# Kernel tuning notes

Hardware: AMD Instinct MI355X
Metric: run time of the kernel (lower is better)

Reference implementation:

```python
import jax, jax.numpy as jnp
import numpy as np


def setup_inputs() -> dict:
    key = jax.random.key(0)
    k1, k2, k3 = jax.random.split(key, 3)
    T, N, D = 128, 2048, 256  # snapshots, nodes, nhid
    inputs = jax.random.normal(k1, (T, N, D), dtype=jnp.float32)
    # torch init: uniform_(-0.1, 0.1)
    weight_W = jax.random.uniform(k2, (D, D), dtype=jnp.float32, minval=-0.1, maxval=0.1)
    weight_proj = jax.random.uniform(k3, (D, 1), dtype=jnp.float32, minval=-0.1, maxval=0.1)
    return {"inputs": inputs, "weight_W": weight_W, "weight_proj": weight_proj,
            "attention_width": 3}


def reference(inputs, weight_W, weight_proj, attention_width):
    # inputs: (T, N, D). For i < w the slice passes through unchanged.
    # For i >= w: window = inputs[i-w:i] (excludes position i),
    #   u = tanh(window @ W)            -> (w, N, D)
    #   a = (u @ proj).squeeze(-1)      -> (w, N)
    #   a = softmax over dim=1 (NODES)  -- legacy nn.Softmax() on 2D input
    #   out_i = sum_w a[...,None] * window -> (N, D)
    T, N, D = inputs.shape
    w = attention_width
    # windows for positions i = w .. T-1: (T-w, w, N, D)
    idx = jnp.arange(T - w)[:, None] + jnp.arange(w)[None, :]
    wins = inputs[idx]
    u = jnp.tanh(jnp.einsum('twnd,de->twne', wins, weight_W))  # (T-w, w, N, D)
    a = jnp.einsum('twnd,d->twn', u, weight_proj[:, 0])        # (T-w, w, N)
    a = jax.nn.softmax(a, axis=2)  # softmax across nodes (faithful to nn.Softmax())
    out = jnp.einsum('twn,twnd->tnd', a, wins)                 # (T-w, N, D)
    return jnp.concatenate([inputs[:w], out], axis=0)          # (T, N, D)
```

## Files before the change

kernel.cpp:

```cpp
#include <hip/hip_runtime.h>
#include <hip/hip_bf16.h>


#define T_DIM 128
#define N_DIM 2048
#define D_DIM 256
#define TS 127
#define M_TOT (TS * N_DIM)
#define BM 256
#define TB 32

typedef __attribute__((ext_vector_type(8))) short bf16x8;
typedef __attribute__((ext_vector_type(4))) float f32x4;

__device__ inline short f2bf(float f) {
  union { float f; unsigned u; } v; v.f = f;
  unsigned r = v.u + 0x7FFFu + ((v.u >> 16) & 1u);
  return (short)(r >> 16);
}

__device__ inline bf16x8 cvt8(const float4 a, const float4 b) {
  bf16x8 r;
  r[0] = f2bf(a.x); r[1] = f2bf(a.y); r[2] = f2bf(a.z); r[3] = f2bf(a.w);
  r[4] = f2bf(b.x); r[5] = f2bf(b.y); r[6] = f2bf(b.z); r[7] = f2bf(b.w);
  return r;
}

__device__ inline float fast_tanh(float x) {
  float e = __expf(fminf(2.0f * x, 30.0f));
  return __fdividef(e - 1.0f, e + 1.0f);
}

__global__ __launch_bounds__(256) void prep_kernel(const float* __restrict__ W,
                                                   short* __restrict__ Wt) {
  int id = blockIdx.x * 256 + threadIdx.x;
  int d = id >> 8;
  int e = id & 255;
  Wt[e * 256 + d] = f2bf(W[d * 256 + e]);
}

__global__ __launch_bounds__(512) void gemm_s_kernel(const float* __restrict__ x,
                                                     const short* __restrict__ Wt,
                                                     const float* __restrict__ proj,
                                                     float* __restrict__ s) {
  __shared__ short Ws[256 * 128];

  const int tid = threadIdx.x;
  const int lane = tid & 63;
  const int w = tid >> 6;
  const int quad = lane >> 4;
  const int l15 = lane & 15;
  const int m0 = blockIdx.x * BM;
  const size_t row0 = (size_t)(m0 + w * 32 + l15);
  const float* xp = x + row0 * D_DIM + quad * 8;
  const int swzc = (l15 & 7) << 4;

  float4 A0[2][2], A1[2][2];
  A0[0][0] = *(const float4*)(xp);
  A0[0][1] = *(const float4*)(xp + 4);
  A0[1][0] = *(const float4*)(xp + 16 * D_DIM);
  A0[1][1] = *(const float4*)(xp + 16 * D_DIM + 4);
  A1[0][0] = *(const float4*)(xp + 32);
  A1[0][1] = *(const float4*)(xp + 36);
  A1[1][0] = *(const float4*)(xp + 32 + 16 * D_DIM);
  A1[1][1] = *(const float4*)(xp + 36 + 16 * D_DIM);

  f32x4 acc[2][16] = {};

#pragma unroll
  for (int half = 0; half < 2; ++half) {
    if (half) __syncthreads();
#pragma unroll
    for (int it = 0; it < 8; ++it) {
      int slot = tid + it * 512;
      int e = slot >> 4;
      int ks = slot & 15;
      uint4 v = *(const uint4*)(Wt + e * D_DIM + half * 128 + ks * 8);
      int dst = (e * 256 + ks * 16) ^ ((e & 7) << 4);
      *(uint4*)((char*)Ws + dst) = v;
    }
    __syncthreads();

#pragma unroll
    for (int kt = 0; kt < 4; ++kt) {
      const int kg = half * 4 + kt;
      bf16x8 a0, a1;
      if ((kg & 1) == 0) {
        a0 = cvt8(A0[0][0], A0[0][1]);
        a1 = cvt8(A0[1][0], A0[1][1]);
        if (kg < 6) {
          const float* q = xp + (kg + 2) * 32;
          A0[0][0] = *(const float4*)(q);
          A0[0][1] = *(const float4*)(q + 4);
          A0[1][0] = *(const float4*)(q + 16 * D_DIM);
          A0[1][1] = *(const float4*)(q + 16 * D_DIM + 4);
        }
      } else {
        a0 = cvt8(A1[0][0], A1[0][1]);
        a1 = cvt8(A1[1][0], A1[1][1]);
        if (kg < 6) {
          const float* q = xp + (kg + 2) * 32;
          A1[0][0] = *(const float4*)(q);
          A1[0][1] = *(const float4*)(q + 4);
          A1[1][0] = *(const float4*)(q + 16 * D_DIM);
          A1[1][1] = *(const float4*)(q + 16 * D_DIM + 4);
        }
      }
      const int kb = (kt * 64 + quad * 16) ^ swzc;
#pragma unroll
      for (int ef = 0; ef < 16; ++ef) {
        const bf16x8 b =
            *(const bf16x8*)((const char*)Ws + (ef * 16 + l15) * 256 + kb);
        acc[0][ef] = __builtin_amdgcn_mfma_f32_16x16x32_bf16(a0, b, acc[0][ef], 0, 0, 0);
        acc[1][ef] = __builtin_amdgcn_mfma_f32_16x16x32_bf16(a1, b, acc[1][ef], 0, 0, 0);
      }
    }
  }

  float pj[16];
#pragma unroll
  for (int ef = 0; ef < 16; ++ef) pj[ef] = proj[ef * 16 + l15];

#pragma unroll
  for (int mf = 0; mf < 2; ++mf) {
#pragma unroll
    for (int r = 0; r < 4; ++r) {
      float val = 0.f;
#pragma unroll
      for (int ef = 0; ef < 16; ++ef)
        val = __builtin_fmaf(fast_tanh(acc[mf][ef][r]), pj[ef], val);
#pragma unroll
      for (int off = 1; off < 16; off <<= 1) val += __shfl_xor(val, off);
      if (l15 == 0) s[m0 + w * 32 + mf * 16 + quad * 4 + r] = val;
    }
  }
}

__global__ __launch_bounds__(256) void softmax_kernel(const float* __restrict__ s,
                                                      float* __restrict__ p) {
  const int t = blockIdx.x;
  const int tid = threadIdx.x;
  const float* row = s + (size_t)t * N_DIM;
  float v[8];
  float mx = -1e30f;
#pragma unroll
  for (int k = 0; k < 8; ++k) {
    v[k] = row[tid + k * 256];
    mx = fmaxf(mx, v[k]);
  }
#pragma unroll
  for (int off = 1; off < 64; off <<= 1) mx = fmaxf(mx, __shfl_xor(mx, off));
  __shared__ float redm[4];
  if ((tid & 63) == 0) redm[tid >> 6] = mx;
  __syncthreads();
  mx = fmaxf(fmaxf(redm[0], redm[1]), fmaxf(redm[2], redm[3]));

  float sum = 0.f;
#pragma unroll
  for (int k = 0; k < 8; ++k) {
    v[k] = __expf(v[k] - mx);
    sum += v[k];
  }
#pragma unroll
  for (int off = 1; off < 64; off <<= 1) sum += __shfl_xor(sum, off);
  __shared__ float reds[4];
  if ((tid & 63) == 0) reds[tid >> 6] = sum;
  __syncthreads();
  sum = reds[0] + reds[1] + reds[2] + reds[3];
  float inv = 1.0f / sum;
#pragma unroll
  for (int k = 0; k < 8; ++k) p[(size_t)t * N_DIM + tid + k * 256] = v[k] * inv;
}

__global__ __launch_bounds__(256) void out_kernel(const float* __restrict__ x,
                                                  const float* __restrict__ p,
                                                  float* __restrict__ out) {
  const int gid = blockIdx.x * 256 + threadIdx.x;
  const int n = gid >> 6;
  const int d4 = gid & 63;
  const int t0 = blockIdx.y * TB;
  const size_t base = (size_t)n * D_DIM + d4 * 4;
  const size_t tstride = (size_t)N_DIM * D_DIM;

  float4 x0 = {}, x1 = {}, x2 = {};
  float p0 = 0.f, p1 = 0.f, p2 = 0.f;
  if (t0 >= 3) {
    x0 = *(const float4*)(x + (t0 - 3) * tstride + base);
    x1 = *(const float4*)(x + (t0 - 2) * tstride + base);
    x2 = *(const float4*)(x + (t0 - 1) * tstride + base);
    p0 = p[(size_t)(t0 - 3) * N_DIM + n];
    p1 = p[(size_t)(t0 - 2) * N_DIM + n];
    p2 = p[(size_t)(t0 - 1) * N_DIM + n];
  }
  for (int t = t0; t < t0 + TB; ++t) {
    const float4 xc = *(const float4*)(x + t * tstride + base);
    const float pc = (t < TS) ? p[(size_t)t * N_DIM + n] : 0.f;
    float4 o;
    if (t >= 3) {
      o.x = p0 * x0.x + p1 * x1.x + p2 * x2.x;
      o.y = p0 * x0.y + p1 * x1.y + p2 * x2.y;
      o.z = p0 * x0.z + p1 * x1.z + p2 * x2.z;
      o.w = p0 * x0.w + p1 * x1.w + p2 * x2.w;
    } else {
      o = xc;
    }
    *(float4*)(out + t * tstride + base) = o;
    x0 = x1; x1 = x2; x2 = xc;
    p0 = p1; p1 = p2; p2 = pc;
  }
}

extern "C" void kernel_launch(void* const* d_in, const int* in_sizes, int n_in,
                              void* d_out, int out_size, void* d_ws, size_t ws_size,
                              hipStream_t stream) {
  const float* x = (const float*)d_in[0];
  const float* W = (const float*)d_in[1];
  const float* proj = (const float*)d_in[2];
  float* out = (float*)d_out;

  char* ws = (char*)d_ws;
  short* Wt = (short*)ws;
  float* s = (float*)(ws + 131072);
  float* p = (float*)(ws + 131072 + 1040384);

  hipLaunchKernelGGL(prep_kernel, dim3(256), dim3(256), 0, stream, W, Wt);

  hipLaunchKernelGGL(gemm_s_kernel, dim3(M_TOT / BM), dim3(512), 0, stream,
                     x, Wt, proj, s);

  hipLaunchKernelGGL(softmax_kernel, dim3(TS), dim3(256), 0, stream, s, p);

  hipLaunchKernelGGL(out_kernel, dim3((N_DIM * 64) / 256, T_DIM / TB), dim3(256), 0,
                     stream, x, p, out);
}
```

Before: 542.3 us.

## Stage full W in LDS, deepen A prefetch, batch loads and nontemporal stores in output

The GEMM kernel now loads the whole bf16 W (128 KB) into shared memory once, dropping the mid-loop sync and reload. It also prefetches four K-slices of activations instead of two and sets launch bounds to two blocks per CU. The output kernel unrolls the time loop by four, issues four x and p loads together, and writes output with nontemporal stores to cut cache pollution. The larger LDS footprint and deeper register prefetch may limit occupancy and could keep two blocks from fitting per CU.

```diff
diff --git a/kernel.cpp b/kernel.cpp
--- a/kernel.cpp
+++ b/kernel.cpp
@@ -39,11 +39,11 @@
   Wt[e * 256 + d] = f2bf(W[d * 256 + e]);
 }
 
-__global__ __launch_bounds__(512) void gemm_s_kernel(const float* __restrict__ x,
-                                                     const short* __restrict__ Wt,
-                                                     const float* __restrict__ proj,
-                                                     float* __restrict__ s) {
-  __shared__ short Ws[256 * 128];
+__global__ __launch_bounds__(512, 2) void gemm_s_kernel(const float* __restrict__ x,
+                                                        const short* __restrict__ Wt,
+                                                        const float* __restrict__ proj,
+                                                        float* __restrict__ s) {
+  __shared__ short Ws[256 * 256];
 
   const int tid = threadIdx.x;
   const int lane = tid & 63;
@@ -55,65 +55,47 @@
   const float* xp = x + row0 * D_DIM + quad * 8;
   const int swzc = (l15 & 7) << 4;
 
-  float4 A0[2][2], A1[2][2];
-  A0[0][0] = *(const float4*)(xp);
-  A0[0][1] = *(const float4*)(xp + 4);
-  A0[1][0] = *(const float4*)(xp + 16 * D_DIM);
-  A0[1][1] = *(const float4*)(xp + 16 * D_DIM + 4);
-  A1[0][0] = *(const float4*)(xp + 32);
-  A1[0][1] = *(const float4*)(xp + 36);
-  A1[1][0] = *(const float4*)(xp + 32 + 16 * D_DIM);
-  A1[1][1] = *(const float4*)(xp + 36 + 16 * D_DIM);
+  float4 A[4][2][2];
+#pragma unroll
+  for (int i = 0; i < 4; ++i) {
+    const float* q = xp + i * 32;
+    A[i][0][0] = *(const float4*)(q);
+    A[i][0][1] = *(const float4*)(q + 4);
+    A[i][1][0] = *(const float4*)(q + 16 * D_DIM);
+    A[i][1][1] = *(const float4*)(q + 16 * D_DIM + 4);
+  }
+
+#pragma unroll
+  for (int it = 0; it < 16; ++it) {
+    int slot = tid + it * 512;
+    int e = slot >> 5;
+    int ks = slot & 31;
+    uint4 v = *(const uint4*)(Wt + e * D_DIM + ks * 8);
+    int dst = e * 512 + ((ks * 16) ^ ((e & 7) << 4));
+    *(uint4*)((char*)Ws + dst) = v;
+  }
+  __syncthreads();
 
   f32x4 acc[2][16] = {};
 
 #pragma unroll
-  for (int half = 0; half < 2; ++half) {
-    if (half) __syncthreads();
-#pragma unroll
-    for (int it = 0; it < 8; ++it) {
-      int slot = tid + it * 512;
-      int e = slot >> 4;
-      int ks = slot & 15;
-      uint4 v = *(const uint4*)(Wt + e * D_DIM + half * 128 + ks * 8);
-      int dst = (e * 256 + ks * 16) ^ ((e & 7) << 4);
-      *(uint4*)((char*)Ws + dst) = v;
+  for (int kg = 0; kg < 8; ++kg) {
+    const bf16x8 a0 = cvt8(A[kg & 3][0][0], A[kg & 3][0][1]);
+    const bf16x8 a1 = cvt8(A[kg & 3][1][0], A[kg & 3][1][1]);
+    if (kg < 4) {
+      const float* q = xp + (kg + 4) * 32;
+      A[kg][0][0] = *(const float4*)(q);
+      A[kg][0][1] = *(const float4*)(q + 4);
+      A[kg][1][0] = *(const float4*)(q + 16 * D_DIM);
+      A[kg][1][1] = *(const float4*)(q + 16 * D_DIM + 4);
     }
-    __syncthreads();
-
-#pragma unroll
-    for (int kt = 0; kt < 4; ++kt) {
-      const int kg = half * 4 + kt;
-      bf16x8 a0, a1;
-      if ((kg & 1) == 0) {
-        a0 = cvt8(A0[0][0], A0[0][1]);
-        a1 = cvt8(A0[1][0], A0[1][1]);
-        if (kg < 6) {
-          const float* q = xp + (kg + 2) * 32;
-          A0[0][0] = *(const float4*)(q);
-          A0[0][1] = *(const float4*)(q + 4);
-          A0[1][0] = *(const float4*)(q + 16 * D_DIM);
-          A0[1][1] = *(const float4*)(q + 16 * D_DIM + 4);
-        }
-      } else {
-        a0 = cvt8(A1[0][0], A1[0][1]);
-        a1 = cvt8(A1[1][0], A1[1][1]);
-        if (kg < 6) {
-          const float* q = xp + (kg + 2) * 32;
-          A1[0][0] = *(const float4*)(q);
-          A1[0][1] = *(const float4*)(q + 4);
-          A1[1][0] = *(const float4*)(q + 16 * D_DIM);
-          A1[1][1] = *(const float4*)(q + 16 * D_DIM + 4);
-        }
-      }
-      const int kb = (kt * 64 + quad * 16) ^ swzc;
-#pragma unroll
-      for (int ef = 0; ef < 16; ++ef) {
-        const bf16x8 b =
-            *(const bf16x8*)((const char*)Ws + (ef * 16 + l15) * 256 + kb);
-        acc[0][ef] = __builtin_amdgcn_mfma_f32_16x16x32_bf16(a0, b, acc[0][ef], 0, 0, 0);
-        acc[1][ef] = __builtin_amdgcn_mfma_f32_16x16x32_bf16(a1, b, acc[1][ef], 0, 0, 0);
-      }
+    const int kb = (kg * 64 + quad * 16) ^ swzc;
+#pragma unroll
+    for (int ef = 0; ef < 16; ++ef) {
+      const bf16x8 b =
+          *(const bf16x8*)((const char*)Ws + (ef * 16 + l15) * 512 + kb);
+      acc[0][ef] = __builtin_amdgcn_mfma_f32_16x16x32_bf16(a0, b, acc[0][ef], 0, 0, 0);
+      acc[1][ef] = __builtin_amdgcn_mfma_f32_16x16x32_bf16(a1, b, acc[1][ef], 0, 0, 0);
     }
   }
 
@@ -192,22 +174,41 @@
     p1 = p[(size_t)(t0 - 2) * N_DIM + n];
     p2 = p[(size_t)(t0 - 1) * N_DIM + n];
   }
-  for (int t = t0; t < t0 + TB; ++t) {
-    const float4 xc = *(const float4*)(x + t * tstride + base);
-    const float pc = (t < TS) ? p[(size_t)t * N_DIM + n] : 0.f;
-    float4 o;
-    if (t >= 3) {
-      o.x = p0 * x0.x + p1 * x1.x + p2 * x2.x;
-      o.y = p0 * x0.y + p1 * x1.y + p2 * x2.y;
-      o.z = p0 * x0.z + p1 * x1.z + p2 * x2.z;
-      o.w = p0 * x0.w + p1 * x1.w + p2 * x2.w;
-    } else {
-      o = xc;
-    }
-    *(float4*)(out + t * tstride + base) = o;
-    x0 = x1; x1 = x2; x2 = xc;
-    p0 = p1; p1 = p2; p2 = pc;
-  }
+
+#define OUT_STEP(C, Q, TT)                                                     \
+  {                                                                            \
+    f32x4 o;                                                                   \
+    if (t + TT >= 3) {                                                         \
+      o[0] = p0 * x0.x + p1 * x1.x + p2 * x2.x;                                \
+      o[1] = p0 * x0.y + p1 * x1.y + p2 * x2.y;                                \
+      o[2] = p0 * x0.z + p1 * x1.z + p2 * x2.z;                                \
+      o[3] = p0 * x0.w + p1 * x1.w + p2 * x2.w;                                \
+    } else {                                                                   \
+      o[0] = C.x; o[1] = C.y; o[2] = C.z; o[3] = C.w;                          \
+    }                                                                          \
+    __builtin_nontemporal_store(                                               \
+        o, (f32x4*)(out + (size_t)(t + TT) * tstride + base));                 \
+    x0 = x1; x1 = x2; x2 = C;                                                  \
+    p0 = p1; p1 = p2; p2 = Q;                                                  \
+  }
+
+#pragma unroll
+  for (int tt = 0; tt < TB; tt += 4) {
+    const int t = t0 + tt;
+    const float4 c0 = *(const float4*)(x + (size_t)(t + 0) * tstride + base);
+    const float4 c1 = *(const float4*)(x + (size_t)(t + 1) * tstride + base);
+    const float4 c2 = *(const float4*)(x + (size_t)(t + 2) * tstride + base);
+    const float4 c3 = *(const float4*)(x + (size_t)(t + 3) * tstride + base);
+    const float q0 = (t + 0 < TS) ? p[(size_t)(t + 0) * N_DIM + n] : 0.f;
+    const float q1 = (t + 1 < TS) ? p[(size_t)(t + 1) * N_DIM + n] : 0.f;
+    const float q2 = (t + 2 < TS) ? p[(size_t)(t + 2) * N_DIM + n] : 0.f;
+    const float q3 = (t + 3 < TS) ? p[(size_t)(t + 3) * N_DIM + n] : 0.f;
+    OUT_STEP(c0, q0, 0)
+    OUT_STEP(c1, q1, 1)
+    OUT_STEP(c2, q2, 2)
+    OUT_STEP(c3, q3, 3)
+  }
+#undef OUT_STEP
 }
 
 extern "C" void kernel_launch(void* const* d_in, const int* in_sizes, int n_in,
```

New measurement: 530.0 us. 1.02x faster.
